# Kernel optimization log

Hardware: AMD Instinct MI355X
Metric: run time of the kernel (lower is better)

## Reference

```python
import jax, jax.numpy as jnp
import numpy as np

RAD2DEG = 180.0 / 3.14159  # module uses 3.14159, not pi

def _conv2d(x, w):
    # x: (N,1,H,W), w: (O,1,3,3), SAME padding, stride 1
    return jax.lax.conv_general_dilated(
        x, w, window_strides=(1, 1), padding='SAME',
        dimension_numbers=('NCHW', 'OIHW', 'NCHW'))

def _make_filters():
    sobel = np.array([[1, 0, -1], [2, 0, -2], [1, 0, -1]], dtype=np.float32)
    f0   = [[0,0,0],[0,1,-1],[0,0,0]]
    f45  = [[0,0,0],[0,1,0],[0,0,-1]]
    f90  = [[0,0,0],[0,1,0],[0,-1,0]]
    f135 = [[0,0,0],[0,1,0],[-1,0,0]]
    f180 = [[0,0,0],[-1,1,0],[0,0,0]]
    f225 = [[-1,0,0],[0,1,0],[0,0,0]]
    f270 = [[0,-1,0],[0,1,0],[0,0,0]]
    f315 = [[0,0,-1],[0,1,0],[0,0,0]]
    dirs = np.stack([f0,f45,f90,f135,f180,f225,f270,f315]).astype(np.float32)
    return sobel, dirs

def setup_inputs() -> dict:
    key = jax.random.key(0)
    H, W = 2160, 3840
    img = jax.random.uniform(key, (1, 3, H, W), dtype=jnp.float32)
    sobel, dirs = _make_filters()
    sobel_h = jnp.asarray(sobel)[None, None]          # (1,1,3,3)
    sobel_v = jnp.asarray(sobel.T)[None, None]        # (1,1,3,3)
    dir_w = jnp.asarray(dirs)[:, None]                # (8,1,3,3)
    return {"img": img, "sobel_h": sobel_h, "sobel_v": sobel_v, "dir_w": dir_w}

def reference(img, sobel_h, sobel_v, dir_w):
    # grayscale: mean of the 3 channels
    gray = (img[:, 0:1] + img[:, 1:2] + img[:, 2:3]) / 3.0        # (1,1,H,W)
    grad_x = _conv2d(gray, sobel_h)
    grad_y = _conv2d(gray, sobel_v)
    grad_mag = jnp.sqrt(grad_x ** 2 + grad_y ** 2)                # (1,1,H,W)
    # orientation in degrees, snapped to multiples of 45 (round-half-even, like torch.round)
    ori = jnp.round((jnp.arctan2(grad_y, grad_x) * RAD2DEG + 180.0) / 45.0)
    idx_pos = jnp.mod(ori, 8.0).astype(jnp.int32)                 # (1,1,H,W)
    idx_neg = jnp.mod(ori + 4.0, 8.0).astype(jnp.int32)
    all_filtered = _conv2d(grad_mag, dir_w)                       # (1,8,H,W)
    # per-pixel channel select (the flattened gather in the original)
    pos = jnp.take_along_axis(all_filtered, idx_pos, axis=1)      # (1,1,H,W)
    neg = jnp.take_along_axis(all_filtered, idx_neg, axis=1)
    is_max = jnp.minimum(pos, neg) > 0.0
    # in-place aliasing in the original: thin_edges/early_threshold alias grad_mag,
    # so the final binary map is: is_max AND (grad_mag >= 0.2)
    th = jnp.where(is_max & (grad_mag >= 0.2), 1.0, 0.0).astype(jnp.float32)
    return th
```

## Files before the change

### kernel.cpp

```cpp
#include <hip/hip_runtime.h>
#include <math.h>

#define IMG_W 3840
#define IMG_H 2160
#define OUTW  120
#define R     20
#define ITERS (R + 4)

#define DXPACK 0x901A
#define DYPACK 0x1A9
#define T1_SLOPE 0.41421317376456f
#define T2_SLOPE 2.41420676743300f
#define SECT_EPS 3.0e-5f
#define FIX_CAP  (1u << 22)

__device__ __noinline__ int slow_sector(float sx, float sy) {
#pragma clang fp contract(off)
    const float RADF = (float)(180.0 / 3.14159);
    float t = atan2f(sy, sx);
    float wv = ((t * RADF) + 180.0f) / 45.0f;
    float ori = rintf(wv);
    float fr = fabsf(wv - ori);
    if (fr > 0.4995f) {
        double td = atan2((double)sy, (double)sx);
        float t2 = (float)td;
        wv = ((t2 * RADF) + 180.0f) / 45.0f;
        ori = rintf(wv);
    }
    return ((int)ori) & 7;
}

__global__ void zero_counter(unsigned* fix) { if (threadIdx.x == 0) fix[0] = 0u; }

__global__ __launch_bounds__(256, 3) void canny_main(const float* __restrict__ img,
                                                     float* __restrict__ out,
                                                     unsigned* __restrict__ fix) {
#pragma clang fp contract(off)
    __shared__ float ring[4 * 512];

    const int lane = threadIdx.x;
    const int wv   = threadIdx.y;
    float* rbase = ring + wv * 512;

    const int strip = blockIdx.x * 4 + wv;
    const int X0 = strip * OUTW;
    const int Y0 = blockIdx.y * R;
    const int r0 = 2 * lane;
    const int x0 = X0 - 2 + r0;
    const int x1 = x0 + 1;
    const bool xk0 = (unsigned)x0 < (unsigned)IMG_W;
    const bool xk1 = (unsigned)x1 < (unsigned)IMG_W;
    const bool outok = (lane >= 1) && (lane <= 60);
    const int  rb = outok ? r0 : 2;
    const int  xc = min(max(x0, 0), IMG_W - 2);

    const float* p0 = img + xc;
    const float* p1 = p0 + (size_t)IMG_W * IMG_H;
    const float* p2 = p1 + (size_t)IMG_W * IMG_H;

    float GL[3], G0[3], G1[3], GR[3];
    float mc0 = 0.f, mc1 = 0.f;
    int dx0 = 0, dy0 = 0, dx1 = 0, dy1 = 0;

#pragma unroll
    for (int k = 0; k < ITERS; ++k) {
        const int y = Y0 - 2 + k;
        const bool yok = (unsigned)y < (unsigned)IMG_H;
        const int yc = min(max(y, 0), IMG_H - 1);
        const size_t o = (size_t)yc * IMG_W;
        const float2 A = *(const float2*)(p0 + o);
        const float2 B = *(const float2*)(p1 + o);
        const float2 C = *(const float2*)(p2 + o);
        float t0 = ((A.x + B.x) + C.x) / 3.0f;
        float t1 = ((A.y + B.y) + C.y) / 3.0f;
        const int s = k % 3;
        float g0 = (yok && xk0) ? t0 : 0.0f;
        float g1 = (yok && xk1) ? t1 : 0.0f;
        G0[s] = g0;
        G1[s] = g1;
        GL[s] = __shfl_up(g1, 1);
        GR[s] = __shfl_down(g0, 1);

        if (k >= 2) {
            const int i0 = (k - 2) % 3, i1 = (k - 1) % 3, i2 = k % 3;
            const int m = y - 1;
            const bool mok = (unsigned)m < (unsigned)IMG_H;

            float sx0 = GL[i0];
            sx0 = sx0 - G1[i0];
            sx0 = sx0 + 2.0f * GL[i1];
            sx0 = sx0 - 2.0f * G1[i1];
            sx0 = sx0 + GL[i2];
            sx0 = sx0 - G1[i2];
            float sy0 = GL[i0];
            sy0 = sy0 + 2.0f * G0[i0];
            sy0 = sy0 + G1[i0];
            sy0 = sy0 - GL[i2];
            sy0 = sy0 - 2.0f * G0[i2];
            sy0 = sy0 - G1[i2];
            float mag0 = sqrtf(sx0 * sx0 + sy0 * sy0);

            float sx1 = G0[i0];
            sx1 = sx1 - GR[i0];
            sx1 = sx1 + 2.0f * G0[i1];
            sx1 = sx1 - 2.0f * GR[i1];
            sx1 = sx1 + G0[i2];
            sx1 = sx1 - GR[i2];
            float sy1 = G0[i0];
            sy1 = sy1 + 2.0f * G1[i0];
            sy1 = sy1 + GR[i0];
            sy1 = sy1 - G0[i2];
            sy1 = sy1 - 2.0f * G1[i2];
            sy1 = sy1 - GR[i2];
            float mag1 = sqrtf(sx1 * sx1 + sy1 * sy1);

            float M0 = (mok && xk0) ? mag0 : 0.0f;
            float M1 = (mok && xk1) ? mag1 : 0.0f;

            float ax0 = fabsf(sx0), ay0 = fabsf(sy0);
            float d10 = fmaf(-T1_SLOPE, ax0, ay0);
            float d20 = fmaf(-T2_SLOPE, ax0, ay0);
            float sA0 = ax0 + ay0;
            int ndx0 = (d20 > 0.0f) ? 0 : ((sx0 > 0.0f) ? -1 : 1);
            int ndy0 = (d10 < 0.0f) ? 0 : ((sy0 > 0.0f) ? -1 : 1);
            bool inb0 = (fabsf(d10) < SECT_EPS * sA0) || (fabsf(d20) < SECT_EPS * sA0);

            float ax1 = fabsf(sx1), ay1 = fabsf(sy1);
            float d11 = fmaf(-T1_SLOPE, ax1, ay1);
            float d21 = fmaf(-T2_SLOPE, ax1, ay1);
            float sA1 = ax1 + ay1;
            int ndx1 = (d21 > 0.0f) ? 0 : ((sx1 > 0.0f) ? -1 : 1);
            int ndy1 = (d11 < 0.0f) ? 0 : ((sy1 > 0.0f) ? -1 : 1);
            bool inb1 = (fabsf(d11) < SECT_EPS * sA1) || (fabsf(d21) < SECT_EPS * sA1);

            bool f0 = inb0 && outok && (M0 >= 0.2f);
            bool f1 = inb1 && outok && (M1 >= 0.2f);
            if (f0 || f1) {
                if (f0) {
                    unsigned id = atomicAdd(fix, 1u);
                    if (id < FIX_CAP) fix[1 + id] = ((unsigned)m << 12) | (unsigned)x0;
                }
                if (f1) {
                    unsigned id = atomicAdd(fix, 1u);
                    if (id < FIX_CAP) fix[1 + id] = ((unsigned)m << 12) | (unsigned)x1;
                }
            }

            float* wr = rbase + ((k - 2) & 3) * 128;
            *(float2*)(wr + r0) = make_float2(M0, M1);

            if (k >= 4) {
                const int n = m - 1;
                float* bA = rbase + ((k - 4) & 3) * 128;
                float* bB = rbase + ((k - 3) & 3) * 128;
                float* bC = rbase + ((k - 2) & 3) * 128;
                float* bp0 = (dy0 < 0) ? bA : ((dy0 > 0) ? bC : bB);
                float* bn0 = (dy0 < 0) ? bC : ((dy0 > 0) ? bA : bB);
                float* bp1 = (dy1 < 0) ? bA : ((dy1 > 0) ? bC : bB);
                float* bn1 = (dy1 < 0) ? bC : ((dy1 > 0) ? bA : bB);
                float mp0 = bp0[rb + dx0];
                float mn0 = bn0[rb - dx0];
                float mp1 = bp1[rb + 1 + dx1];
                float mn1 = bn1[rb + 1 - dx1];
                float r0v = (fminf(mc0 - mp0, mc0 - mn0) > 0.0f && mc0 >= 0.2f) ? 1.0f : 0.0f;
                float r1v = (fminf(mc1 - mp1, mc1 - mn1) > 0.0f && mc1 >= 0.2f) ? 1.0f : 0.0f;
                if (outok)
                    *(float2*)(out + (size_t)n * IMG_W + x0) = make_float2(r0v, r1v);
            }
            mc0 = M0; mc1 = M1;
            dx0 = ndx0; dy0 = ndy0; dx1 = ndx1; dy1 = ndy1;
        }
    }
}

__device__ __forceinline__ float gray_at(const float* img, int xx, int yy) {
#pragma clang fp contract(off)
    if ((unsigned)xx >= (unsigned)IMG_W || (unsigned)yy >= (unsigned)IMG_H) return 0.0f;
    size_t o = (size_t)yy * IMG_W + xx;
    float c0 = img[o];
    float c1 = img[o + (size_t)IMG_W * IMG_H];
    float c2 = img[o + 2 * (size_t)IMG_W * IMG_H];
    return ((c0 + c1) + c2) / 3.0f;
}

__device__ void sobel_at(const float* img, int xx, int yy, float& sxo, float& syo) {
#pragma clang fp contract(off)
    float a00 = gray_at(img, xx - 1, yy - 1), a01 = gray_at(img, xx, yy - 1), a02 = gray_at(img, xx + 1, yy - 1);
    float a10 = gray_at(img, xx - 1, yy),                                     a12 = gray_at(img, xx + 1, yy);
    float a20 = gray_at(img, xx - 1, yy + 1), a21 = gray_at(img, xx, yy + 1), a22 = gray_at(img, xx + 1, yy + 1);
    float s = a00;
    s = s - a02;
    s = s + 2.0f * a10;
    s = s - 2.0f * a12;
    s = s + a20;
    s = s - a22;
    sxo = s;
    float t = a00;
    t = t + 2.0f * a01;
    t = t + a02;
    t = t - a20;
    t = t - 2.0f * a21;
    t = t - a22;
    syo = t;
}

__device__ float mag_at(const float* img, int xx, int yy) {
#pragma clang fp contract(off)
    if ((unsigned)xx >= (unsigned)IMG_W || (unsigned)yy >= (unsigned)IMG_H) return 0.0f;
    float sx, sy;
    sobel_at(img, xx, yy, sx, sy);
    return sqrtf(sx * sx + sy * sy);
}

__global__ void canny_fixup(const float* __restrict__ img, float* __restrict__ out,
                            const unsigned* __restrict__ fix) {
#pragma clang fp contract(off)
    unsigned cnt = fix[0];
    if (cnt > FIX_CAP) cnt = FIX_CAP;
    for (unsigned i = blockIdx.x * blockDim.x + threadIdx.x; i < cnt;
         i += gridDim.x * blockDim.x) {
        unsigned pk = fix[1 + i];
        int xx = (int)(pk & 4095u), yy = (int)(pk >> 12);
        float sx, sy;
        sobel_at(img, xx, yy, sx, sy);
        int idx = slow_sector(sx, sy);
        int dxo = ((DXPACK >> (2 * idx)) & 3) - 1;
        int dyo = ((DYPACK >> (2 * idx)) & 3) - 1;
        float mc = sqrtf(sx * sx + sy * sy);
        float mp = mag_at(img, xx + dxo, yy + dyo);
        float mn = mag_at(img, xx - dxo, yy - dyo);
        out[(size_t)yy * IMG_W + xx] =
            (fminf(mc - mp, mc - mn) > 0.0f && mc >= 0.2f) ? 1.0f : 0.0f;
    }
}

extern "C" void kernel_launch(void* const* d_in, const int* in_sizes, int n_in,
                              void* d_out, int out_size, void* d_ws, size_t ws_size,
                              hipStream_t stream) {
    const float* img = (const float*)d_in[0];
    float* out = (float*)d_out;
    unsigned* fix = (unsigned*)d_ws;
    zero_counter<<<1, 64, 0, stream>>>(fix);
    canny_main<<<dim3(8, IMG_H / R), dim3(64, 4), 0, stream>>>(img, out, fix);
    canny_fixup<<<dim3(16), dim3(256), 0, stream>>>(img, out, fix);
}
```

Baseline: 188.6 us.

## Fuse fixup into main kernel with per-wave LDS fix lists and squared magnitudes

Merges the zero-counter, main and fixup kernels into one launch. Ambiguous pixels now go into per-wave shared-memory lists instead of a global atomic list, and each wave recomputes them itself at the end. Squared magnitudes replace sqrt in the main path, with extra tie and threshold bands sent to the exact fixup. Input rows are software-prefetched P rows ahead, and the 4-row LDS ring becomes a full strip buffer. The cost is more shared memory and registers, which may lower occupancy, plus a capped per-wave fix list that could overflow.

```diff
diff --git a/kernel.cpp b/kernel.cpp
--- a/kernel.cpp
+++ b/kernel.cpp
@@ -6,171 +6,33 @@
 #define OUTW  120
 #define R     20
 #define ITERS (R + 4)
+#define P     3
+#define MROWS (R + 2)
+#define CAP   224
 
 #define DXPACK 0x901A
 #define DYPACK 0x1A9
 #define T1_SLOPE 0.41421317376456f
 #define T2_SLOPE 2.41420676743300f
-#define SECT_EPS 3.0e-5f
-#define FIX_CAP  (1u << 22)
-
-__device__ __noinline__ int slow_sector(float sx, float sy) {
+#define SECT_EPS  3.0e-5f
+#define QE        0.04f
+#define QBAND_EPS 1.0e-4f
+#define TIE_EPS   1.0e-4f
+
+__device__ __forceinline__ int slow_sector(float sx, float sy) {
 #pragma clang fp contract(off)
     const float RADF = (float)(180.0 / 3.14159);
     float t = atan2f(sy, sx);
-    float wv = ((t * RADF) + 180.0f) / 45.0f;
-    float ori = rintf(wv);
-    float fr = fabsf(wv - ori);
+    float wvv = ((t * RADF) + 180.0f) / 45.0f;
+    float ori = rintf(wvv);
+    float fr = fabsf(wvv - ori);
     if (fr > 0.4995f) {
         double td = atan2((double)sy, (double)sx);
         float t2 = (float)td;
-        wv = ((t2 * RADF) + 180.0f) / 45.0f;
-        ori = rintf(wv);
+        wvv = ((t2 * RADF) + 180.0f) / 45.0f;
+        ori = rintf(wvv);
     }
     return ((int)ori) & 7;
-}
-
-__global__ void zero_counter(unsigned* fix) { if (threadIdx.x == 0) fix[0] = 0u; }
-
-__global__ __launch_bounds__(256, 3) void canny_main(const float* __restrict__ img,
-                                                     float* __restrict__ out,
-                                                     unsigned* __restrict__ fix) {
-#pragma clang fp contract(off)
-    __shared__ float ring[4 * 512];
-
-    const int lane = threadIdx.x;
-    const int wv   = threadIdx.y;
-    float* rbase = ring + wv * 512;
-
-    const int strip = blockIdx.x * 4 + wv;
-    const int X0 = strip * OUTW;
-    const int Y0 = blockIdx.y * R;
-    const int r0 = 2 * lane;
-    const int x0 = X0 - 2 + r0;
-    const int x1 = x0 + 1;
-    const bool xk0 = (unsigned)x0 < (unsigned)IMG_W;
-    const bool xk1 = (unsigned)x1 < (unsigned)IMG_W;
-    const bool outok = (lane >= 1) && (lane <= 60);
-    const int  rb = outok ? r0 : 2;
-    const int  xc = min(max(x0, 0), IMG_W - 2);
-
-    const float* p0 = img + xc;
-    const float* p1 = p0 + (size_t)IMG_W * IMG_H;
-    const float* p2 = p1 + (size_t)IMG_W * IMG_H;
-
-    float GL[3], G0[3], G1[3], GR[3];
-    float mc0 = 0.f, mc1 = 0.f;
-    int dx0 = 0, dy0 = 0, dx1 = 0, dy1 = 0;
-
-#pragma unroll
-    for (int k = 0; k < ITERS; ++k) {
-        const int y = Y0 - 2 + k;
-        const bool yok = (unsigned)y < (unsigned)IMG_H;
-        const int yc = min(max(y, 0), IMG_H - 1);
-        const size_t o = (size_t)yc * IMG_W;
-        const float2 A = *(const float2*)(p0 + o);
-        const float2 B = *(const float2*)(p1 + o);
-        const float2 C = *(const float2*)(p2 + o);
-        float t0 = ((A.x + B.x) + C.x) / 3.0f;
-        float t1 = ((A.y + B.y) + C.y) / 3.0f;
-        const int s = k % 3;
-        float g0 = (yok && xk0) ? t0 : 0.0f;
-        float g1 = (yok && xk1) ? t1 : 0.0f;
-        G0[s] = g0;
-        G1[s] = g1;
-        GL[s] = __shfl_up(g1, 1);
-        GR[s] = __shfl_down(g0, 1);
-
-        if (k >= 2) {
-            const int i0 = (k - 2) % 3, i1 = (k - 1) % 3, i2 = k % 3;
-            const int m = y - 1;
-            const bool mok = (unsigned)m < (unsigned)IMG_H;
-
-            float sx0 = GL[i0];
-            sx0 = sx0 - G1[i0];
-            sx0 = sx0 + 2.0f * GL[i1];
-            sx0 = sx0 - 2.0f * G1[i1];
-            sx0 = sx0 + GL[i2];
-            sx0 = sx0 - G1[i2];
-            float sy0 = GL[i0];
-            sy0 = sy0 + 2.0f * G0[i0];
-            sy0 = sy0 + G1[i0];
-            sy0 = sy0 - GL[i2];
-            sy0 = sy0 - 2.0f * G0[i2];
-            sy0 = sy0 - G1[i2];
-            float mag0 = sqrtf(sx0 * sx0 + sy0 * sy0);
-
-            float sx1 = G0[i0];
-            sx1 = sx1 - GR[i0];
-            sx1 = sx1 + 2.0f * G0[i1];
-            sx1 = sx1 - 2.0f * GR[i1];
-            sx1 = sx1 + G0[i2];
-            sx1 = sx1 - GR[i2];
-            float sy1 = G0[i0];
-            sy1 = sy1 + 2.0f * G1[i0];
-            sy1 = sy1 + GR[i0];
-            sy1 = sy1 - G0[i2];
-            sy1 = sy1 - 2.0f * G1[i2];
-            sy1 = sy1 - GR[i2];
-            float mag1 = sqrtf(sx1 * sx1 + sy1 * sy1);
-
-            float M0 = (mok && xk0) ? mag0 : 0.0f;
-            float M1 = (mok && xk1) ? mag1 : 0.0f;
-
-            float ax0 = fabsf(sx0), ay0 = fabsf(sy0);
-            float d10 = fmaf(-T1_SLOPE, ax0, ay0);
-            float d20 = fmaf(-T2_SLOPE, ax0, ay0);
-            float sA0 = ax0 + ay0;
-            int ndx0 = (d20 > 0.0f) ? 0 : ((sx0 > 0.0f) ? -1 : 1);
-            int ndy0 = (d10 < 0.0f) ? 0 : ((sy0 > 0.0f) ? -1 : 1);
-            bool inb0 = (fabsf(d10) < SECT_EPS * sA0) || (fabsf(d20) < SECT_EPS * sA0);
-
-            float ax1 = fabsf(sx1), ay1 = fabsf(sy1);
-            float d11 = fmaf(-T1_SLOPE, ax1, ay1);
-            float d21 = fmaf(-T2_SLOPE, ax1, ay1);
-            float sA1 = ax1 + ay1;
-            int ndx1 = (d21 > 0.0f) ? 0 : ((sx1 > 0.0f) ? -1 : 1);
-            int ndy1 = (d11 < 0.0f) ? 0 : ((sy1 > 0.0f) ? -1 : 1);
-            bool inb1 = (fabsf(d11) < SECT_EPS * sA1) || (fabsf(d21) < SECT_EPS * sA1);
-
-            bool f0 = inb0 && outok && (M0 >= 0.2f);
-            bool f1 = inb1 && outok && (M1 >= 0.2f);
-            if (f0 || f1) {
-                if (f0) {
-                    unsigned id = atomicAdd(fix, 1u);
-                    if (id < FIX_CAP) fix[1 + id] = ((unsigned)m << 12) | (unsigned)x0;
-                }
-                if (f1) {
-                    unsigned id = atomicAdd(fix, 1u);
-                    if (id < FIX_CAP) fix[1 + id] = ((unsigned)m << 12) | (unsigned)x1;
-                }
-            }
-
-            float* wr = rbase + ((k - 2) & 3) * 128;
-            *(float2*)(wr + r0) = make_float2(M0, M1);
-
-            if (k >= 4) {
-                const int n = m - 1;
-                float* bA = rbase + ((k - 4) & 3) * 128;
-                float* bB = rbase + ((k - 3) & 3) * 128;
-                float* bC = rbase + ((k - 2) & 3) * 128;
-                float* bp0 = (dy0 < 0) ? bA : ((dy0 > 0) ? bC : bB);
-                float* bn0 = (dy0 < 0) ? bC : ((dy0 > 0) ? bA : bB);
-                float* bp1 = (dy1 < 0) ? bA : ((dy1 > 0) ? bC : bB);
-                float* bn1 = (dy1 < 0) ? bC : ((dy1 > 0) ? bA : bB);
-                float mp0 = bp0[rb + dx0];
-                float mn0 = bn0[rb - dx0];
-                float mp1 = bp1[rb + 1 + dx1];
-                float mn1 = bn1[rb + 1 - dx1];
-                float r0v = (fminf(mc0 - mp0, mc0 - mn0) > 0.0f && mc0 >= 0.2f) ? 1.0f : 0.0f;
-                float r1v = (fminf(mc1 - mp1, mc1 - mn1) > 0.0f && mc1 >= 0.2f) ? 1.0f : 0.0f;
-                if (outok)
-                    *(float2*)(out + (size_t)n * IMG_W + x0) = make_float2(r0v, r1v);
-            }
-            mc0 = M0; mc1 = M1;
-            dx0 = ndx0; dy0 = ndy0; dx1 = ndx1; dy1 = ndy1;
-        }
-    }
 }
 
 __device__ __forceinline__ float gray_at(const float* img, int xx, int yy) {
@@ -212,21 +74,153 @@
     return sqrtf(sx * sx + sy * sy);
 }
 
-__global__ void canny_fixup(const float* __restrict__ img, float* __restrict__ out,
-                            const unsigned* __restrict__ fix) {
-#pragma clang fp contract(off)
-    unsigned cnt = fix[0];
-    if (cnt > FIX_CAP) cnt = FIX_CAP;
-    for (unsigned i = blockIdx.x * blockDim.x + threadIdx.x; i < cnt;
-         i += gridDim.x * blockDim.x) {
-        unsigned pk = fix[1 + i];
+__global__ __launch_bounds__(256, 3) void canny_main(const float* __restrict__ img,
+                                                     float* __restrict__ out) {
+    __shared__ float strip[4][MROWS][128];
+    __shared__ unsigned fixl[4][CAP];
+    __shared__ unsigned fixn[4];
+
+    const int lane = threadIdx.x;
+    const int wv   = threadIdx.y;
+    float* sbase = &strip[wv][0][0];
+    unsigned* flist = fixl[wv];
+    if (lane == 0) fixn[wv] = 0u;
+
+    const int X0 = (blockIdx.x * 4 + wv) * OUTW;
+    const int Y0 = blockIdx.y * R;
+    const int r0 = 2 * lane;
+    const int x0i = X0 - 2 + r0;
+    const int x1i = x0i + 1;
+    const bool xk0 = (unsigned)x0i < (unsigned)IMG_W;
+    const bool xk1 = (unsigned)x1i < (unsigned)IMG_W;
+    const bool outok = (lane >= 1) && (lane <= 60);
+    const int rb = outok ? r0 : 2;
+    const int xc = min(max(x0i, 0), IMG_W - 2);
+
+    const float* p0 = img + xc;
+    const float* p1 = p0 + (size_t)IMG_W * IMG_H;
+    const float* p2 = p1 + (size_t)IMG_W * IMG_H;
+
+    float2 rA[P], rB[P], rC[P];
+#pragma unroll
+    for (int j = 0; j < P; ++j) {
+        int yc = min(max(Y0 - 2 + j, 0), IMG_H - 1);
+        size_t o = (size_t)yc * IMG_W;
+        rA[j] = *(const float2*)(p0 + o);
+        rB[j] = *(const float2*)(p1 + o);
+        rC[j] = *(const float2*)(p2 + o);
+    }
+
+    const float INV3 = 1.0f / 3.0f;
+    float GL[3], G0[3], G1[3], GR[3];
+    float mq0 = 0.f, mq1 = 0.f;
+    int off0 = 0, off1 = 0;
+    bool bnd0 = false, bnd1 = false;
+
+#pragma unroll
+    for (int k = 0; k < ITERS; ++k) {
+        const int y = Y0 - 2 + k;
+        const bool yok = (unsigned)y < (unsigned)IMG_H;
+        const int sl = k % P;
+        float2 A = rA[sl], B = rB[sl], C = rC[sl];
+        if (k + P < ITERS) {
+            int yc2 = min(max(y + P, 0), IMG_H - 1);
+            size_t o2 = (size_t)yc2 * IMG_W;
+            rA[sl] = *(const float2*)(p0 + o2);
+            rB[sl] = *(const float2*)(p1 + o2);
+            rC[sl] = *(const float2*)(p2 + o2);
+        }
+        float g0 = (yok && xk0) ? ((A.x + B.x) + C.x) * INV3 : 0.0f;
+        float g1 = (yok && xk1) ? ((A.y + B.y) + C.y) * INV3 : 0.0f;
+        const int s = k % 3;
+        G0[s] = g0; G1[s] = g1;
+        GL[s] = __shfl_up(g1, 1);
+        GR[s] = __shfl_down(g0, 1);
+
+        if (k >= 2) {
+            const int i0 = (k - 2) % 3, i1 = (k - 1) % 3, i2 = k % 3;
+            const int m = y - 1;
+            const bool mok = (unsigned)m < (unsigned)IMG_H;
+
+            float sx0 = GL[i0] - G1[i0] + 2.0f * (GL[i1] - G1[i1]) + GL[i2] - G1[i2];
+            float sy0 = GL[i0] + 2.0f * G0[i0] + G1[i0] - GL[i2] - 2.0f * G0[i2] - G1[i2];
+            float q0v = sx0 * sx0 + sy0 * sy0;
+            float sx1 = G0[i0] - GR[i0] + 2.0f * (G0[i1] - GR[i1]) + G0[i2] - GR[i2];
+            float sy1 = G0[i0] + 2.0f * G1[i0] + GR[i0] - G0[i2] - 2.0f * G1[i2] - GR[i2];
+            float q1v = sx1 * sx1 + sy1 * sy1;
+
+            const bool v0 = mok && xk0, v1 = mok && xk1;
+            float Q0 = v0 ? q0v : 0.0f;
+            float Q1 = v1 ? q1v : 0.0f;
+
+            float ax0 = fabsf(sx0), ay0 = fabsf(sy0);
+            float d10 = fmaf(-T1_SLOPE, ax0, ay0);
+            float d20 = fmaf(-T2_SLOPE, ax0, ay0);
+            float sA0 = ax0 + ay0;
+            int ndx0 = (d20 > 0.0f) ? 0 : ((sx0 > 0.0f) ? -1 : 1);
+            int ndy0 = (d10 < 0.0f) ? 0 : ((sy0 > 0.0f) ? -1 : 1);
+            bool nb0 = (fabsf(d10) < SECT_EPS * sA0) || (fabsf(d20) < SECT_EPS * sA0)
+                     || (fabsf(q0v - QE) <= QBAND_EPS * (q0v + QE));
+
+            float ax1 = fabsf(sx1), ay1 = fabsf(sy1);
+            float d11 = fmaf(-T1_SLOPE, ax1, ay1);
+            float d21 = fmaf(-T2_SLOPE, ax1, ay1);
+            float sA1 = ax1 + ay1;
+            int ndx1 = (d21 > 0.0f) ? 0 : ((sx1 > 0.0f) ? -1 : 1);
+            int ndy1 = (d11 < 0.0f) ? 0 : ((sy1 > 0.0f) ? -1 : 1);
+            bool nb1 = (fabsf(d11) < SECT_EPS * sA1) || (fabsf(d21) < SECT_EPS * sA1)
+                     || (fabsf(q1v - QE) <= QBAND_EPS * (q1v + QE));
+
+            *(float2*)(sbase + (k - 2) * 128 + r0) = make_float2(Q0, Q1);
+
+            if (k >= 4) {
+                float* cp0 = sbase + (k - 3) * 128 + rb;
+                float* cp1 = cp0 + 1;
+                float mp0 = cp0[off0], mn0 = cp0[-off0];
+                float mp1 = cp1[off1], mn1 = cp1[-off1];
+                float r0v = (mq0 > mp0 && mq0 > mn0 && mq0 >= QE) ? 1.0f : 0.0f;
+                float r1v = (mq1 > mp1 && mq1 > mn1 && mq1 >= QE) ? 1.0f : 0.0f;
+                if (outok)
+                    *(float2*)(out + (size_t)(Y0 + k - 4) * IMG_W + x0i) = make_float2(r0v, r1v);
+                bool cand0 = mq0 >= QE * (1.0f - 3.0f * QBAND_EPS);
+                bool cand1 = mq1 >= QE * (1.0f - 3.0f * QBAND_EPS);
+                bool tie0 = (fabsf(mq0 - mp0) <= TIE_EPS * (mq0 + mp0)) ||
+                            (fabsf(mq0 - mn0) <= TIE_EPS * (mq0 + mn0));
+                bool tie1 = (fabsf(mq1 - mp1) <= TIE_EPS * (mq1 + mp1)) ||
+                            (fabsf(mq1 - mn1) <= TIE_EPS * (mq1 + mn1));
+                bool f0 = outok && cand0 && (bnd0 || tie0);
+                bool f1 = outok && cand1 && (bnd1 || tie1);
+                if (f0 || f1) {
+                    int n = Y0 + k - 4;
+                    if (f0) {
+                        unsigned id = atomicAdd(&fixn[wv], 1u);
+                        if (id < CAP) flist[id] = ((unsigned)n << 12) | (unsigned)x0i;
+                    }
+                    if (f1) {
+                        unsigned id = atomicAdd(&fixn[wv], 1u);
+                        if (id < CAP) flist[id] = ((unsigned)n << 12) | (unsigned)x1i;
+                    }
+                }
+            }
+            mq0 = Q0; mq1 = Q1;
+            off0 = v0 ? (ndy0 * 128 + ndx0) : 0;
+            off1 = v1 ? (ndy1 * 128 + ndx1) : 0;
+            bnd0 = nb0; bnd1 = nb1;
+        }
+    }
+
+    __threadfence();
+    unsigned n = fixn[wv];
+    if (n > CAP) n = CAP;
+    for (unsigned i = lane; i < n; i += 64) {
+        unsigned pk = flist[i];
         int xx = (int)(pk & 4095u), yy = (int)(pk >> 12);
         float sx, sy;
         sobel_at(img, xx, yy, sx, sy);
         int idx = slow_sector(sx, sy);
         int dxo = ((DXPACK >> (2 * idx)) & 3) - 1;
         int dyo = ((DYPACK >> (2 * idx)) & 3) - 1;
-        float mc = sqrtf(sx * sx + sy * sy);
+        float mc = mag_at(img, xx, yy);
         float mp = mag_at(img, xx + dxo, yy + dyo);
         float mn = mag_at(img, xx - dxo, yy - dyo);
         out[(size_t)yy * IMG_W + xx] =
@@ -239,8 +233,5 @@
                               hipStream_t stream) {
     const float* img = (const float*)d_in[0];
     float* out = (float*)d_out;
-    unsigned* fix = (unsigned*)d_ws;
-    zero_counter<<<1, 64, 0, stream>>>(fix);
-    canny_main<<<dim3(8, IMG_H / R), dim3(64, 4), 0, stream>>>(img, out, fix);
-    canny_fixup<<<dim3(16), dim3(256), 0, stream>>>(img, out, fix);
-}
+    canny_main<<<dim3(8, IMG_H / R), dim3(64, 4), 0, stream>>>(img, out);
+}
```

Result: slower. 300.3 us (+59.3%).
